# Kernel optimization log

Hardware: AMD Instinct MI355X
Metric: run time of the kernel (lower is better)

The kernel has to match this reference:

```python
import jax, jax.numpy as jnp
import numpy as np

HEADS = 2
C1 = 33    # per-head out channels, conv1
C2 = 550   # per-head out channels, conv2


def _lin_params(key, fan_in, fan_out):
    kw, kb = jax.random.split(key)
    scale = 1.0 / np.sqrt(fan_in)
    W = jax.random.uniform(kw, (fan_in, fan_out), jnp.float32, -scale, scale)
    b = jax.random.uniform(kb, (fan_out,), jnp.float32, -scale, scale)
    return W, b


def transformer_conv(x, src, dst, Wq, bq, Wk, bk, Wv, bv, Ws, bs, heads, out_ch):
    """PyG TransformerConv (concat=True, root_weight=True, beta=False)."""
    N = x.shape[0]
    q = (x @ Wq + bq).reshape(N, heads, out_ch)  # query of target node i
    k = (x @ Wk + bk).reshape(N, heads, out_ch)  # key of source node j
    v = (x @ Wv + bv).reshape(N, heads, out_ch)  # value of source node j
    # attention logits per edge: [E, H]
    alpha = jnp.einsum('ehc,ehc->eh', q[dst], k[src]) / jnp.sqrt(jnp.float32(out_ch))
    # segment softmax over incoming edges of each dst node
    m = jax.lax.stop_gradient(jax.ops.segment_max(alpha, dst, num_segments=N))  # [N,H]
    e = jnp.exp(alpha - m[dst])
    denom = jax.ops.segment_sum(e, dst, num_segments=N)  # [N,H]
    a = e / denom[dst]
    # weighted scatter-aggregate of source values: [N,H,C]
    out = jax.ops.segment_sum(a[..., None] * v[src], dst, num_segments=N)
    out = out.reshape(N, heads * out_ch)
    # root/skip connection
    out = out + x @ Ws + bs
    return out


def setup_inputs() -> dict:
    key = jax.random.key(0)
    ks = jax.random.split(key, 10)
    N, E, IN = 20000, 120000, 256
    x = jax.random.normal(ks[0], (N, IN), jnp.float32)
    edge_index = jax.random.randint(ks[1], (2, E), 0, N, jnp.int64 if jax.config.jax_enable_x64 else jnp.int32)
    d = {'x': x, 'edge_index': edge_index}
    # conv1: IN -> heads*C1
    d['Wq1'], d['bq1'] = _lin_params(ks[2], IN, HEADS * C1)
    d['Wk1'], d['bk1'] = _lin_params(ks[3], IN, HEADS * C1)
    d['Wv1'], d['bv1'] = _lin_params(ks[4], IN, HEADS * C1)
    d['Ws1'], d['bs1'] = _lin_params(ks[5], IN, HEADS * C1)
    # conv2: heads*C1 -> heads*C2
    IN2 = HEADS * C1
    d['Wq2'], d['bq2'] = _lin_params(ks[6], IN2, HEADS * C2)
    d['Wk2'], d['bk2'] = _lin_params(ks[7], IN2, HEADS * C2)
    d['Wv2'], d['bv2'] = _lin_params(ks[8], IN2, HEADS * C2)
    d['Ws2'], d['bs2'] = _lin_params(ks[9], IN2, HEADS * C2)
    return d


def reference(x, edge_index, Wq1, bq1, Wk1, bk1, Wv1, bv1, Ws1, bs1,
              Wq2, bq2, Wk2, bk2, Wv2, bv2, Ws2, bs2):
    src, dst = edge_index[0], edge_index[1]
    h = transformer_conv(x, src, dst, Wq1, bq1, Wk1, bk1, Wv1, bv1, Ws1, bs1, HEADS, C1)
    h = transformer_conv(h, src, dst, Wq2, bq2, Wk2, bk2, Wv2, bv2, Ws2, bs2, HEADS, C2)
    # x.view(N, 550, heads).max(dim=2) -- faithful to the original reshape layout
    h = h.reshape(h.shape[0], C2, HEADS)
    return jnp.max(h, axis=2)
```

## Files before the change

kernel.cpp:

```cpp
#include <hip/hip_runtime.h>
#include <math.h>

#define HEADS 2
#define C1    33
#define C2    550
#define D1    66
#define D2    1100
#define IN1   256
#define PROJW 288
#define KU    224
#define N2P   1152
#define KZ    96
#define ZW    144

typedef __attribute__((ext_vector_type(8))) short bfrag;
typedef __attribute__((ext_vector_type(4))) float f32x4;

__device__ inline unsigned short f2bf(float f) {
    unsigned int u = __float_as_uint(f);
    u += 0x7FFFu + ((u >> 16) & 1u);
    return (unsigned short)(u >> 16);
}

__device__ inline int xcd_slot(int bid, int slots) {
    return (bid >> 3) + (bid & 7) * slots;
}

__global__ void k_cvt(const float* __restrict__ x, unsigned short* __restrict__ xb, int total4) {
    int i = blockIdx.x * blockDim.x + threadIdx.x;
    if (i >= total4) return;
    float4 v = ((const float4*)x)[i];
    ushort4 o;
    o.x = f2bf(v.x); o.y = f2bf(v.y); o.z = f2bf(v.z); o.w = f2bf(v.w);
    ((ushort4*)xb)[i] = o;
}

__global__ void k_prep1(const float* __restrict__ Wq, const float* __restrict__ bq,
                        const float* __restrict__ Wk, const float* __restrict__ bk,
                        const float* __restrict__ Wv, const float* __restrict__ bv,
                        const float* __restrict__ Ws, const float* __restrict__ bs,
                        unsigned short* __restrict__ Wt1, float* __restrict__ bcat) {
    int bid = blockIdx.x;
    int lk = bid & 3, t = bid >> 2;
    int ks = t & 7, g = t >> 3;
    int col = threadIdx.x;
    int c = g * 96 + col;
    int k0 = ks * 32 + lk * 8;
    short vals[8];
    float bia = 0.f;
    if (c < 4 * D1) {
        int m = c / D1, j = c % D1;
        const float* W; const float* B;
        switch (m) {
            case 0: W = Wq; B = bq; break;
            case 1: W = Wk; B = bk; break;
            case 2: W = Wv; B = bv; break;
            default: W = Ws; B = bs; break;
        }
        #pragma unroll
        for (int e = 0; e < 8; e++) vals[e] = (short)f2bf(W[(size_t)(k0 + e) * D1 + j]);
        bia = B[j];
    } else {
        #pragma unroll
        for (int e = 0; e < 8; e++) vals[e] = 0;
    }
    *(bfrag*)&Wt1[((size_t)bid * 96 + col) * 8] = *(bfrag*)vals;
    if (ks == 0 && lk == 0) bcat[c] = bia;
}

__global__ void k_prep2(const float* __restrict__ Wv2, const float* __restrict__ bv2,
                        const float* __restrict__ Ws2, const float* __restrict__ bs2,
                        unsigned short* __restrict__ W2t,
                        float* __restrict__ bvp, float* __restrict__ bsp) {
    int bid = blockIdx.x;
    int lk = bid & 3, t = bid >> 2;
    int ks = t % 7, g = t / 7;
    int col = threadIdx.x;
    int c = g * 96 + col;
    int k0 = ks * 32 + lk * 8;
    short vals[8];
    #pragma unroll
    for (int e = 0; e < 8; e++) {
        int k = k0 + e;
        float val = 0.f;
        if (c < D2) {
            if (c < C2) {
                if (k < 66) val = Wv2[(size_t)k * D2 + c];
                else if (k >= 132 && k < 198) val = Ws2[(size_t)(k - 132) * D2 + c];
            } else {
                if (k >= 66 && k < 132) val = Wv2[(size_t)(k - 66) * D2 + c];
                else if (k >= 132 && k < 198) val = Ws2[(size_t)(k - 132) * D2 + c];
            }
        }
        vals[e] = (short)f2bf(val);
    }
    *(bfrag*)&W2t[((size_t)bid * 96 + col) * 8] = *(bfrag*)vals;
    if (ks == 0 && lk == 0) {
        bvp[c] = (c < D2) ? bv2[c] : 0.f;
        bsp[c] = (c < D2) ? bs2[c] : 0.f;
    }
}

__global__ void k_hist(const int* __restrict__ dst, int E, int* __restrict__ cnt) {
    int e = blockIdx.x * blockDim.x + threadIdx.x;
    if (e < E) atomicAdd(&cnt[dst[e]], 1);
}

__global__ void k_scan(const int* __restrict__ cnt, int* __restrict__ roff,
                       int* __restrict__ pos, int N) {
    __shared__ int wsum[16];
    __shared__ int carry_s;
    int tid = threadIdx.x, wid = tid >> 6, lane = tid & 63;
    if (tid == 0) { carry_s = 0; roff[0] = 0; }
    __syncthreads();
    for (int base = 0; base < N; base += 1024) {
        int i = base + tid;
        int v = (i < N) ? cnt[i] : 0;
        int x = v;
        #pragma unroll
        for (int s = 1; s < 64; s <<= 1) {
            int t = __shfl_up(x, s, 64);
            if (lane >= s) x += t;
        }
        if (lane == 63) wsum[wid] = x;
        __syncthreads();
        if (tid < 16) {
            int y = wsum[tid];
            #pragma unroll
            for (int s = 1; s < 16; s <<= 1) {
                int t = __shfl_up(y, s, 16);
                if (tid >= s) y += t;
            }
            wsum[tid] = y;
        }
        __syncthreads();
        int carry = carry_s;
        int incl = carry + (wid ? wsum[wid - 1] : 0) + x;
        if (i < N) { roff[i + 1] = incl; pos[i] = incl - v; }
        __syncthreads();
        if (tid == 0) carry_s = carry + wsum[15];
        __syncthreads();
    }
}

__global__ void k_fill(const int* __restrict__ src, const int* __restrict__ dst, int E,
                       int* __restrict__ pos, int* __restrict__ elist) {
    int e = blockIdx.x * blockDim.x + threadIdx.x;
    if (e < E) {
        int slot = atomicAdd(&pos[dst[e]], 1);
        elist[slot] = src[e];
    }
}

__global__ __launch_bounds__(256) void k_mm1(
        const unsigned short* __restrict__ A, const unsigned short* __restrict__ B,
        const float* __restrict__ bias, float* __restrict__ proj, int N,
        int nRow, int slots) {
    int s = xcd_slot(blockIdx.x, slots);
    if (s >= nRow * 3) return;
    int rowt = s / 3, g = s - rowt * 3;
    int cbase = g * 96;
    int wave = threadIdx.x >> 6, lane = threadIdx.x & 63;
    int lr = lane & 15, lk = lane >> 4;
    int rbase = rowt * 128 + wave * 32;
    int ar[2];
    #pragma unroll
    for (int mi = 0; mi < 2; mi++) {
        int r = rbase + mi * 16 + lr;
        ar[mi] = (r < N) ? r : (N - 1);
    }
    bfrag a[2][8];
    #pragma unroll
    for (int mi = 0; mi < 2; mi++)
        #pragma unroll
        for (int ks = 0; ks < 8; ks++)
            a[mi][ks] = *(const bfrag*)(A + (size_t)ar[mi] * IN1 + ks * 32 + lk * 8);
    f32x4 acc[2][6];
    #pragma unroll
    for (int mi = 0; mi < 2; mi++)
        #pragma unroll
        for (int ni = 0; ni < 6; ni++) acc[mi][ni] = (f32x4){0.f, 0.f, 0.f, 0.f};
    #pragma unroll
    for (int ks = 0; ks < 8; ks++) {
        bfrag b[6];
        #pragma unroll
        for (int ni = 0; ni < 6; ni++)
            b[ni] = *(const bfrag*)(B + (size_t)(g * 8 + ks) * 3072 + lk * 768 + (ni * 16 + lr) * 8);
        #pragma unroll
        for (int mi = 0; mi < 2; mi++)
            #pragma unroll
            for (int ni = 0; ni < 6; ni++)
                acc[mi][ni] = __builtin_amdgcn_mfma_f32_16x16x32_bf16(a[mi][ks], b[ni], acc[mi][ni], 0, 0, 0);
    }
    #pragma unroll
    for (int mi = 0; mi < 2; mi++) {
        #pragma unroll
        for (int ni = 0; ni < 6; ni++) {
            int col = cbase + ni * 16 + lr;
            float bia = bias[col];
            #pragma unroll
            for (int r = 0; r < 4; r++) {
                int row = rbase + mi * 16 + lk * 4 + r;
                if (row < N) proj[(size_t)row * PROJW + col] = acc[mi][ni][r] + bia;
            }
        }
    }
}

__global__ __launch_bounds__(128) void k_conv1(
        const float* __restrict__ proj, const int* __restrict__ roff,
        const int* __restrict__ elist, float* __restrict__ h1,
        unsigned short* __restrict__ h1b, int N) {
    int n = blockIdx.x;
    int h = threadIdx.x >> 6;
    int lane = threadIdx.x & 63;
    size_t pb = (size_t)n * PROJW;
    int hc = h * C1;
    bool ok = (lane < C1);
    float my_q = ok ? proj[pb + hc + lane] : 0.f;
    float s1v  = ok ? proj[pb + 198 + hc + lane] : 0.f;
    float m = -INFINITY, lsum = 0.f, acc = 0.f;
    int e0 = roff[n], e1 = roff[n + 1];
    const float isc = 0.17407765595569785f;
    int e = e0;
    for (; e + 3 < e1; e += 4) {
        int s0 = elist[e], s1 = elist[e + 1], s2 = elist[e + 2], s3 = elist[e + 3];
        size_t b0 = (size_t)s0 * PROJW, b1 = (size_t)s1 * PROJW;
        size_t b2 = (size_t)s2 * PROJW, b3 = (size_t)s3 * PROJW;
        float k0 = ok ? proj[b0 + 66 + hc + lane] : 0.f;
        float k1 = ok ? proj[b1 + 66 + hc + lane] : 0.f;
        float k2 = ok ? proj[b2 + 66 + hc + lane] : 0.f;
        float k3 = ok ? proj[b3 + 66 + hc + lane] : 0.f;
        float v0 = ok ? proj[b0 + 132 + hc + lane] : 0.f;
        float v1 = ok ? proj[b1 + 132 + hc + lane] : 0.f;
        float v2 = ok ? proj[b2 + 132 + hc + lane] : 0.f;
        float v3 = ok ? proj[b3 + 132 + hc + lane] : 0.f;
        float p0 = my_q * k0, p1 = my_q * k1, p2 = my_q * k2, p3 = my_q * k3;
        #pragma unroll
        for (int off = 32; off >= 1; off >>= 1) {
            p0 += __shfl_xor(p0, off, 64);
            p1 += __shfl_xor(p1, off, 64);
            p2 += __shfl_xor(p2, off, 64);
            p3 += __shfl_xor(p3, off, 64);
        }
        float a0 = p0 * isc, a1 = p1 * isc, a2 = p2 * isc, a3 = p3 * isc;
        float mp = fmaxf(fmaxf(a0, a1), fmaxf(a2, a3));
        float e0v = __expf(a0 - mp), e1v = __expf(a1 - mp);
        float e2v = __expf(a2 - mp), e3v = __expf(a3 - mp);
        float lp = (e0v + e1v) + (e2v + e3v);
        float ap = (e0v * v0 + e1v * v1) + (e2v * v2 + e3v * v3);
        float mnew = fmaxf(m, mp);
        float sc = __expf(m - mnew), sp = __expf(mp - mnew);
        lsum = lsum * sc + lp * sp;
        acc  = acc * sc + ap * sp;
        m = mnew;
    }
    for (; e + 1 < e1; e += 2) {
        int sa = elist[e], sb = elist[e + 1];
        size_t ba = (size_t)sa * PROJW, bb = (size_t)sb * PROJW;
        float ka = ok ? proj[ba + 66 + hc + lane] : 0.f;
        float va = ok ? proj[ba + 132 + hc + lane] : 0.f;
        float kb = ok ? proj[bb + 66 + hc + lane] : 0.f;
        float vb = ok ? proj[bb + 132 + hc + lane] : 0.f;
        float pa = my_q * ka, pbv = my_q * kb;
        #pragma unroll
        for (int off = 32; off >= 1; off >>= 1) {
            pa  += __shfl_xor(pa, off, 64);
            pbv += __shfl_xor(pbv, off, 64);
        }
        float aa = pa * isc, ab = pbv * isc;
        float mp = fmaxf(aa, ab);
        float ea = __expf(aa - mp), eb = __expf(ab - mp);
        float lp = ea + eb, ap = ea * va + eb * vb;
        float mnew = fmaxf(m, mp);
        float sc = __expf(m - mnew), sp = __expf(mp - mnew);
        lsum = lsum * sc + lp * sp;
        acc  = acc * sc + ap * sp;
        m = mnew;
    }
    if (e < e1) {
        int s = elist[e];
        size_t sb = (size_t)s * PROJW;
        float kv = ok ? proj[sb + 66 + hc + lane] : 0.f;
        float vv = ok ? proj[sb + 132 + hc + lane] : 0.f;
        float prod = my_q * kv;
        #pragma unroll
        for (int off = 32; off >= 1; off >>= 1) prod += __shfl_xor(prod, off, 64);
        float alpha = prod * isc;
        float mnew = fmaxf(m, alpha);
        float sc = __expf(m - mnew);
        float p = __expf(alpha - mnew);
        lsum = lsum * sc + p;
        acc  = acc * sc + p * vv;
        m = mnew;
    }
    if (ok) {
        float res = (lsum > 0.f) ? acc / lsum : 0.f;
        float val = res + s1v;
        h1[(size_t)n * D1 + hc + lane] = val;
        h1b[(size_t)n * KZ + hc + lane] = f2bf(val);
    } else if (h == 1 && lane >= C1 && lane < C1 + 30) {
        h1b[(size_t)n * KZ + D1 + (lane - C1)] = 0;
    }
}

__global__ __launch_bounds__(256) void k_precomp(
        const float* __restrict__ Wq2, const float* __restrict__ bq2,
        const float* __restrict__ Wk2, const float* __restrict__ bk2,
        float* __restrict__ G, float* __restrict__ wqbk,
        float* __restrict__ wkbq, float* __restrict__ cc) {
    int wave = threadIdx.x >> 6, lane = threadIdx.x & 63;
    int j = blockIdx.x * 4 + wave;
    if (j >= 8978) return;
    const float *u, *v;
    float* outp;
    if (j < 8976) {
        int h = j / 4488;
        int r = j % 4488;
        int a = r / 68, b = r % 68;
        if (b < 66)      { u = Wq2 + (size_t)a * D2 + h * C2; v = Wk2 + (size_t)b * D2 + h * C2; outp = &G[h * 4356 + a * 66 + b]; }
        else if (b == 66){ u = Wq2 + (size_t)a * D2 + h * C2; v = bk2 + h * C2;                  outp = &wqbk[h * 66 + a]; }
        else             { u = Wk2 + (size_t)a * D2 + h * C2; v = bq2 + h * C2;                  outp = &wkbq[h * 66 + a]; }
    } else {
        int h = j - 8976;
        u = bq2 + h * C2; v = bk2 + h * C2; outp = &cc[h];
    }
    float acc = 0.f;
    for (int c = lane; c < C2; c += 64) acc += u[c] * v[c];
    #pragma unroll
    for (int off = 32; off >= 1; off >>= 1) acc += __shfl_xor(acc, off, 64);
    if (lane == 0) *outp = acc;
}

__global__ void k_prepz(const float* __restrict__ G, const float* __restrict__ wqbk,
                        const float* __restrict__ wkbq, unsigned short* __restrict__ GBt) {
    int bid = blockIdx.x;
    int lk = bid & 3, t = bid >> 2;
    int ks = t % 3, g = t / 3;
    int col = threadIdx.x;
    int r = g * 96 + col;
    int k0 = ks * 32 + lk * 8;
    short vals[8];
    #pragma unroll
    for (int e = 0; e < 8; e++) {
        int k = k0 + e;
        float v = 0.f;
        if (k < D1) {
            if (r < 132) v = G[r * D1 + k];
            else if (r < 134) v = wqbk[(r - 132) * D1 + k];
            else if (r < 136) v = wkbq[(r - 134) * D1 + k];
        }
        vals[e] = (short)f2bf(v);
    }
    *(bfrag*)&GBt[((size_t)bid * 96 + col) * 8] = *(bfrag*)vals;
}

__global__ __launch_bounds__(256) void k_mmz(
        const unsigned short* __restrict__ A, const unsigned short* __restrict__ B,
        float* __restrict__ Z, int N, int nRow, int slots) {
    int s = xcd_slot(blockIdx.x, slots);
    if (s >= nRow * 2) return;
    int rowt = s >> 1, g = s & 1;
    int wave = threadIdx.x >> 6, lane = threadIdx.x & 63;
    int lr = lane & 15, lk = lane >> 4;
    int rbase = rowt * 64 + (wave >> 1) * 32;
    int ch = (wave & 1) * 48;
    int cbase = g * 96 + ch;
    f32x4 acc[2][3];
    #pragma unroll
    for (int i = 0; i < 2; i++)
        #pragma unroll
        for (int j = 0; j < 3; j++) acc[i][j] = (f32x4){0.f, 0.f, 0.f, 0.f};
    int ar[2];
    #pragma unroll
    for (int mi = 0; mi < 2; mi++) {
        int r = rbase + mi * 16 + lr;
        ar[mi] = (r < N) ? r : (N - 1);
    }
    #pragma unroll
    for (int ks = 0; ks < 3; ks++) {
        bfrag a[2], b[3];
        #pragma unroll
        for (int mi = 0; mi < 2; mi++)
            a[mi] = *(const bfrag*)(A + (size_t)ar[mi] * KZ + ks * 32 + lk * 8);
        #pragma unroll
        for (int ni = 0; ni < 3; ni++)
            b[ni] = *(const bfrag*)(B + (size_t)(g * 3 + ks) * 3072 + lk * 768 + (ch + ni * 16 + lr) * 8);
        #pragma unroll
        for (int mi = 0; mi < 2; mi++)
            #pragma unroll
            for (int ni = 0; ni < 3; ni++)
                acc[mi][ni] = __builtin_amdgcn_mfma_f32_16x16x32_bf16(a[mi], b[ni], acc[mi][ni], 0, 0, 0);
    }
    #pragma unroll
    for (int mi = 0; mi < 2; mi++) {
        #pragma unroll
        for (int ni = 0; ni < 3; ni++) {
            int col = cbase + ni * 16 + lr;
            if (col >= 136) continue;
            #pragma unroll
            for (int r = 0; r < 4; r++) {
                int row = rbase + mi * 16 + lk * 4 + r;
                if (row < N) Z[(size_t)row * ZW + col] = acc[mi][ni][r];
            }
        }
    }
}

__global__ __launch_bounds__(128) void k_conv2(
        const float* __restrict__ h1, const float* __restrict__ Z,
        const float* __restrict__ cc, const int* __restrict__ roff,
        const int* __restrict__ elist, unsigned short* __restrict__ U,
        float* __restrict__ flag, int N) {
    int n = blockIdx.x;
    int h = threadIdx.x >> 6;
    int lane = threadIdx.x & 63;
    int c0 = lane, c1 = lane + 64;
    bool ok1 = (c1 < D1);
    float hd0 = h1[(size_t)n * D1 + c0];
    float hd1 = ok1 ? h1[(size_t)n * D1 + c1] : 0.f;
    float adv = Z[(size_t)n * ZW + 132 + h] + cc[h];
    float m = -INFINITY, lsum = 0.f, a0 = 0.f, a1 = 0.f;
    int e0 = roff[n], e1 = roff[n + 1];
    const float isc = 0.04264014327112209f;
    int hD = h * D1;
    int e = e0;
    for (; e + 3 < e1; e += 4) {
        int s0 = elist[e], s1 = elist[e + 1], s2 = elist[e + 2], s3 = elist[e + 3];
        const float* z0 = Z + (size_t)s0 * ZW;
        const float* z1 = Z + (size_t)s1 * ZW;
        const float* z2 = Z + (size_t)s2 * ZW;
        const float* z3 = Z + (size_t)s3 * ZW;
        float p0 = hd0 * z0[hD + c0] + (ok1 ? hd1 * z0[hD + c1] : 0.f);
        float p1 = hd0 * z1[hD + c0] + (ok1 ? hd1 * z1[hD + c1] : 0.f);
        float p2 = hd0 * z2[hD + c0] + (ok1 ? hd1 * z2[hD + c1] : 0.f);
        float p3 = hd0 * z3[hD + c0] + (ok1 ? hd1 * z3[hD + c1] : 0.f);
        #pragma unroll
        for (int off = 32; off >= 1; off >>= 1) {
            p0 += __shfl_xor(p0, off, 64);
            p1 += __shfl_xor(p1, off, 64);
            p2 += __shfl_xor(p2, off, 64);
            p3 += __shfl_xor(p3, off, 64);
        }
        float al0 = (p0 + adv + z0[134 + h]) * isc;
        float al1 = (p1 + adv + z1[134 + h]) * isc;
        float al2 = (p2 + adv + z2[134 + h]) * isc;
        float al3 = (p3 + adv + z3[134 + h]) * isc;
        float va00 = h1[(size_t)s0 * D1 + c0];
        float va01 = ok1 ? h1[(size_t)s0 * D1 + c1] : 0.f;
        float va10 = h1[(size_t)s1 * D1 + c0];
        float va11 = ok1 ? h1[(size_t)s1 * D1 + c1] : 0.f;
        float va20 = h1[(size_t)s2 * D1 + c0];
        float va21 = ok1 ? h1[(size_t)s2 * D1 + c1] : 0.f;
        float va30 = h1[(size_t)s3 * D1 + c0];
        float va31 = ok1 ? h1[(size_t)s3 * D1 + c1] : 0.f;
        float mp = fmaxf(fmaxf(al0, al1), fmaxf(al2, al3));
        float e0v = __expf(al0 - mp), e1v = __expf(al1 - mp);
        float e2v = __expf(al2 - mp), e3v = __expf(al3 - mp);
        float lp = (e0v + e1v) + (e2v + e3v);
        float ap0 = (e0v * va00 + e1v * va10) + (e2v * va20 + e3v * va30);
        float ap1 = (e0v * va01 + e1v * va11) + (e2v * va21 + e3v * va31);
        float mnew = fmaxf(m, mp);
        float sc = __expf(m - mnew), sp = __expf(mp - mnew);
        lsum = lsum * sc + lp * sp;
        a0 = a0 * sc + ap0 * sp;
        a1 = a1 * sc + ap1 * sp;
        m = mnew;
    }
    for (; e + 1 < e1; e += 2) {
        int sa = elist[e], sb = elist[e + 1];
        const float* za = Z + (size_t)sa * ZW;
        const float* zb = Z + (size_t)sb * ZW;
        float pa = hd0 * za[hD + c0] + (ok1 ? hd1 * za[hD + c1] : 0.f);
        float pb = hd0 * zb[hD + c0] + (ok1 ? hd1 * zb[hD + c1] : 0.f);
        #pragma unroll
        for (int off = 32; off >= 1; off >>= 1) {
            pa += __shfl_xor(pa, off, 64);
            pb += __shfl_xor(pb, off, 64);
        }
        float aa = (pa + adv + za[134 + h]) * isc;
        float ab = (pb + adv + zb[134 + h]) * isc;
        float va0 = h1[(size_t)sa * D1 + c0];
        float va1 = ok1 ? h1[(size_t)sa * D1 + c1] : 0.f;
        float vb0 = h1[(size_t)sb * D1 + c0];
        float vb1 = ok1 ? h1[(size_t)sb * D1 + c1] : 0.f;
        float mp = fmaxf(aa, ab);
        float ea = __expf(aa - mp), eb = __expf(ab - mp);
        float lp = ea + eb;
        float ap0 = ea * va0 + eb * vb0;
        float ap1 = ea * va1 + eb * vb1;
        float mnew = fmaxf(m, mp);
        float sc = __expf(m - mnew), sp = __expf(mp - mnew);
        lsum = lsum * sc + lp * sp;
        a0 = a0 * sc + ap0 * sp;
        a1 = a1 * sc + ap1 * sp;
        m = mnew;
    }
    if (e < e1) {
        int s = elist[e];
        const float* zr = Z + (size_t)s * ZW;
        float prod = hd0 * zr[hD + c0] + (ok1 ? hd1 * zr[hD + c1] : 0.f);
        #pragma unroll
        for (int off = 32; off >= 1; off >>= 1) prod += __shfl_xor(prod, off, 64);
        float alpha = (prod + adv + zr[134 + h]) * isc;
        float mnew = fmaxf(m, alpha);
        float sc = __expf(m - mnew);
        float p = __expf(alpha - mnew);
        lsum = lsum * sc + p;
        float v0 = h1[(size_t)s * D1 + c0];
        float vv1 = ok1 ? h1[(size_t)s * D1 + c1] : 0.f;
        a0 = a0 * sc + p * v0;
        a1 = a1 * sc + p * vv1;
        m = mnew;
    }
    float inv = (lsum > 0.f) ? 1.f / lsum : 0.f;
    size_t ub = (size_t)n * KU;
    U[ub + hD + c0] = f2bf(a0 * inv);
    if (ok1) U[ub + hD + c1] = f2bf(a1 * inv);
    if (h == 0) {
        U[ub + 132 + c0] = f2bf(hd0);
        if (ok1) U[ub + 132 + c1] = f2bf(hd1);
    } else if (lane < KU - 198) {
        U[ub + 198 + lane] = 0;
    }
    if (lane == 0) flag[n * 2 + h] = (lsum > 0.f) ? 1.f : 0.f;
}

__global__ __launch_bounds__(256) void k_mm2(
        const unsigned short* __restrict__ A, const unsigned short* __restrict__ B,
        const float* __restrict__ bvp, const float* __restrict__ bsp,
        const float* __restrict__ flag, float* __restrict__ out, int N,
        int nRow, int slots) {
    int s = xcd_slot(blockIdx.x, slots);
    if (s >= nRow * 12) return;
    int rowt = s / 12, g = s - rowt * 12;
    int cbase = g * 96;
    int wave = threadIdx.x >> 6, lane = threadIdx.x & 63;
    int lr = lane & 15, lk = lane >> 4;
    int rbase = rowt * 128 + wave * 32;
    int ar[2];
    #pragma unroll
    for (int mi = 0; mi < 2; mi++) {
        int r = rbase + mi * 16 + lr;
        ar[mi] = (r < N) ? r : (N - 1);
    }
    bfrag a[2][7];
    #pragma unroll
    for (int mi = 0; mi < 2; mi++)
        #pragma unroll
        for (int ks = 0; ks < 7; ks++)
            a[mi][ks] = *(const bfrag*)(A + (size_t)ar[mi] * KU + ks * 32 + lk * 8);
    f32x4 acc[2][6];
    #pragma unroll
    for (int mi = 0; mi < 2; mi++)
        #pragma unroll
        for (int ni = 0; ni < 6; ni++) acc[mi][ni] = (f32x4){0.f, 0.f, 0.f, 0.f};
    #pragma unroll
    for (int ks = 0; ks < 7; ks++) {
        bfrag b[6];
        #pragma unroll
        for (int ni = 0; ni < 6; ni++)
            b[ni] = *(const bfrag*)(B + (size_t)(g * 7 + ks) * 3072 + lk * 768 + (ni * 16 + lr) * 8);
        #pragma unroll
        for (int mi = 0; mi < 2; mi++)
            #pragma unroll
            for (int ni = 0; ni < 6; ni++)
                acc[mi][ni] = __builtin_amdgcn_mfma_f32_16x16x32_bf16(a[mi][ks], b[ni], acc[mi][ni], 0, 0, 0);
    }
    #pragma unroll
    for (int mi = 0; mi < 2; mi++) {
        #pragma unroll
        for (int ni = 0; ni < 6; ni++) {
            int col = cbase + ni * 16 + lr;
            float bv = bvp[col], bs_ = bsp[col];
            int hh = (col >= C2) ? 1 : 0;
            #pragma unroll
            for (int r = 0; r < 4; r++) {
                int row = rbase + mi * 16 + lk * 4 + r;
                int fr = (row < N) ? row : 0;
                float val = acc[mi][ni][r] + flag[fr * 2 + hh] * bv + bs_;
                float oth = __shfl_xor(val, 1, 64);
                if (row < N && col < D2 && !(col & 1))
                    out[(size_t)row * C2 + (col >> 1)] = fmaxf(val, oth);
            }
        }
    }
}

extern "C" void kernel_launch(void* const* d_in, const int* in_sizes, int n_in,
                              void* d_out, int out_size, void* d_ws, size_t ws_size,
                              hipStream_t stream) {
    const float* x  = (const float*)d_in[0];
    const int*   ei = (const int*)d_in[1];
    int N = in_sizes[0] / IN1;
    int E = in_sizes[1] / 2;
    const int* src = ei;
    const int* dst = ei + E;

    const float *Wq1 = (const float*)d_in[2],  *bq1 = (const float*)d_in[3];
    const float *Wk1 = (const float*)d_in[4],  *bk1 = (const float*)d_in[5];
    const float *Wv1 = (const float*)d_in[6],  *bv1 = (const float*)d_in[7];
    const float *Ws1 = (const float*)d_in[8],  *bs1 = (const float*)d_in[9];
    const float *Wq2 = (const float*)d_in[10], *bq2 = (const float*)d_in[11];
    const float *Wk2 = (const float*)d_in[12], *bk2 = (const float*)d_in[13];
    const float *Wv2 = (const float*)d_in[14], *bv2 = (const float*)d_in[15];
    const float *Ws2 = (const float*)d_in[16], *bs2 = (const float*)d_in[17];

    char* w = (char*)d_ws;
    size_t off = 0;
    auto take = [&](size_t bytes) { size_t o = off; off = (off + bytes + 255) & ~(size_t)255; return o; };

    unsigned short* xb = (unsigned short*)(w + take((size_t)N * IN1 * 2));
    size_t proj_off = take((size_t)N * PROJW * 4);
    float* proj = (float*)(w + proj_off);
    float* Z = proj;
    unsigned short* U = (unsigned short*)(w + proj_off + (size_t)N * ZW * 4);
    float* h1   = (float*)(w + take((size_t)N * D1 * 4));
    unsigned short* h1b = (unsigned short*)(w + take((size_t)N * KZ * 2));
    float* flag = (float*)(w + take((size_t)N * 2 * 4));
    float* G    = (float*)(w + take((size_t)2 * D1 * D1 * 4));
    float* wqbk = (float*)(w + take(2 * D1 * 4));
    float* wkbq = (float*)(w + take(2 * D1 * 4));
    float* cc   = (float*)(w + take(2 * 4));
    unsigned short* GBt = (unsigned short*)(w + take((size_t)24 * 96 * 8 * 2));
    unsigned short* Wt1 = (unsigned short*)(w + take((size_t)96 * 96 * 8 * 2));
    float* bcat = (float*)(w + take(PROJW * 4));
    unsigned short* W2t = (unsigned short*)(w + take((size_t)336 * 96 * 8 * 2));
    float* bvp  = (float*)(w + take(N2P * 4));
    float* bsp  = (float*)(w + take(N2P * 4));
    int* cnt   = (int*)(w + take((size_t)N * 4));
    int* roff  = (int*)(w + take((size_t)(N + 1) * 4));
    int* pos   = (int*)(w + take((size_t)N * 4));
    int* elist = (int*)(w + take((size_t)E * 4));

    hipMemsetAsync(cnt, 0, (size_t)N * sizeof(int), stream);
    k_hist<<<(E + 255) / 256, 256, 0, stream>>>(dst, E, cnt);
    k_scan<<<1, 1024, 0, stream>>>(cnt, roff, pos, N);
    k_fill<<<(E + 255) / 256, 256, 0, stream>>>(src, dst, E, pos, elist);

    k_cvt<<<(N * IN1 / 4 + 255) / 256, 256, 0, stream>>>(x, xb, N * IN1 / 4);
    k_prep1<<<96, 96, 0, stream>>>(Wq1, bq1, Wk1, bk1, Wv1, bv1, Ws1, bs1, Wt1, bcat);
    k_prep2<<<336, 96, 0, stream>>>(Wv2, bv2, Ws2, bs2, W2t, bvp, bsp);
    k_precomp<<<(8978 + 3) / 4, 256, 0, stream>>>(Wq2, bq2, Wk2, bk2, G, wqbk, wkbq, cc);
    k_prepz<<<24, 96, 0, stream>>>(G, wqbk, wkbq, GBt);

    int nRow1 = (N + 127) / 128;
    int tot1  = nRow1 * 3;
    int slots1 = (tot1 + 7) / 8;
    int nRowZ = (N + 63) / 64;
    int totZ  = nRowZ * 2;
    int slotsZ = (totZ + 7) / 8;
    int nRow2 = (N + 127) / 128;
    int tot2  = nRow2 * 12;
    int slots2 = (tot2 + 7) / 8;

    k_mm1<<<slots1 * 8, 256, 0, stream>>>(xb, Wt1, bcat, proj, N, nRow1, slots1);
    k_conv1<<<N, 128, 0, stream>>>(proj, roff, elist, h1, h1b, N);

    k_mmz<<<slotsZ * 8, 256, 0, stream>>>(h1b, GBt, Z, N, nRowZ, slotsZ);

    k_conv2<<<N, 128, 0, stream>>>(h1, Z, cc, roff, elist, U, flag, N);

    k_mm2<<<slots2 * 8, 256, 0, stream>>>(U, W2t, bvp, bsp, flag, (float*)d_out, N, nRow2, slots2);
}
```

Before: 192.5 us.

## Fold conv2 biases into padded K columns and stage mm2 output through LDS

The value and skip biases of the second layer move into spare K rows of the packed weight matrix. Matching indicator columns are written into U: a per-head flag for rows that have incoming edges, plus a constant one. This removes the separate flag buffer and the per-element bias loads from the mm2 epilogue. The epilogue now writes the head-max results into shared memory and stores them as contiguous row segments, replacing scattered strided stores. Biases now pass through bf16 rounding, which adds a little precision loss.

```diff
diff --git a/kernel.cpp b/kernel.cpp
--- a/kernel.cpp
+++ b/kernel.cpp
@@ -70,8 +70,7 @@
 
 __global__ void k_prep2(const float* __restrict__ Wv2, const float* __restrict__ bv2,
                         const float* __restrict__ Ws2, const float* __restrict__ bs2,
-                        unsigned short* __restrict__ W2t,
-                        float* __restrict__ bvp, float* __restrict__ bsp) {
+                        unsigned short* __restrict__ W2t) {
     int bid = blockIdx.x;
     int lk = bid & 3, t = bid >> 2;
     int ks = t % 7, g = t / 7;
@@ -87,18 +86,18 @@
             if (c < C2) {
                 if (k < 66) val = Wv2[(size_t)k * D2 + c];
                 else if (k >= 132 && k < 198) val = Ws2[(size_t)(k - 132) * D2 + c];
+                else if (k == 198) val = bv2[c];
+                else if (k == 223) val = bs2[c];
             } else {
                 if (k >= 66 && k < 132) val = Wv2[(size_t)(k - 66) * D2 + c];
                 else if (k >= 132 && k < 198) val = Ws2[(size_t)(k - 132) * D2 + c];
+                else if (k == 199) val = bv2[c];
+                else if (k == 223) val = bs2[c];
             }
         }
         vals[e] = (short)f2bf(val);
     }
     *(bfrag*)&W2t[((size_t)bid * 96 + col) * 8] = *(bfrag*)vals;
-    if (ks == 0 && lk == 0) {
-        bvp[c] = (c < D2) ? bv2[c] : 0.f;
-        bsp[c] = (c < D2) ? bs2[c] : 0.f;
-    }
 }
 
 __global__ void k_hist(const int* __restrict__ dst, int E, int* __restrict__ cnt) {
@@ -410,8 +409,7 @@
 __global__ __launch_bounds__(128) void k_conv2(
         const float* __restrict__ h1, const float* __restrict__ Z,
         const float* __restrict__ cc, const int* __restrict__ roff,
-        const int* __restrict__ elist, unsigned short* __restrict__ U,
-        float* __restrict__ flag, int N) {
+        const int* __restrict__ elist, unsigned short* __restrict__ U, int N) {
     int n = blockIdx.x;
     int h = threadIdx.x >> 6;
     int lane = threadIdx.x & 63;
@@ -517,24 +515,23 @@
     size_t ub = (size_t)n * KU;
     U[ub + hD + c0] = f2bf(a0 * inv);
     if (ok1) U[ub + hD + c1] = f2bf(a1 * inv);
+    if (lane == 0) U[ub + 198 + h] = (lsum > 0.f) ? (unsigned short)0x3F80 : (unsigned short)0;
     if (h == 0) {
         U[ub + 132 + c0] = f2bf(hd0);
         if (ok1) U[ub + 132 + c1] = f2bf(hd1);
-    } else if (lane < KU - 198) {
-        U[ub + 198 + lane] = 0;
-    }
-    if (lane == 0) flag[n * 2 + h] = (lsum > 0.f) ? 1.f : 0.f;
+        if (lane == 1) U[ub + 223] = (unsigned short)0x3F80;
+    } else if (lane >= 34 && lane < 57) {
+        U[ub + 200 + (lane - 34)] = 0;
+    }
 }
 
 __global__ __launch_bounds__(256) void k_mm2(
         const unsigned short* __restrict__ A, const unsigned short* __restrict__ B,
-        const float* __restrict__ bvp, const float* __restrict__ bsp,
-        const float* __restrict__ flag, float* __restrict__ out, int N,
-        int nRow, int slots) {
+        float* __restrict__ out, int N, int nRow, int slots) {
+    __shared__ float ot[4][32][49];
     int s = xcd_slot(blockIdx.x, slots);
     if (s >= nRow * 12) return;
     int rowt = s / 12, g = s - rowt * 12;
-    int cbase = g * 96;
     int wave = threadIdx.x >> 6, lane = threadIdx.x & 63;
     int lr = lane & 15, lk = lane >> 4;
     int rbase = rowt * 128 + wave * 32;
@@ -571,19 +568,25 @@
     for (int mi = 0; mi < 2; mi++) {
         #pragma unroll
         for (int ni = 0; ni < 6; ni++) {
-            int col = cbase + ni * 16 + lr;
-            float bv = bvp[col], bs_ = bsp[col];
-            int hh = (col >= C2) ? 1 : 0;
             #pragma unroll
             for (int r = 0; r < 4; r++) {
-                int row = rbase + mi * 16 + lk * 4 + r;
-                int fr = (row < N) ? row : 0;
-                float val = acc[mi][ni][r] + flag[fr * 2 + hh] * bv + bs_;
+                float val = acc[mi][ni][r];
                 float oth = __shfl_xor(val, 1, 64);
-                if (row < N && col < D2 && !(col & 1))
-                    out[(size_t)row * C2 + (col >> 1)] = fmaxf(val, oth);
+                if (!(lane & 1))
+                    ot[wave][mi * 16 + lk * 4 + r][ni * 8 + (lr >> 1)] = fmaxf(val, oth);
             }
         }
+    }
+    __syncthreads();
+    int colb = g * 48;
+    #pragma unroll
+    for (int i = 0; i < 24; i++) {
+        int t = i * 64 + lane;
+        int r32 = t / 48, pos = t - r32 * 48;
+        int row = rbase + r32;
+        int col = colb + pos;
+        if (row < N && col < C2)
+            out[(size_t)row * C2 + col] = ot[wave][r32][pos];
     }
 }
 
@@ -617,7 +620,6 @@
     unsigned short* U = (unsigned short*)(w + proj_off + (size_t)N * ZW * 4);
     float* h1   = (float*)(w + take((size_t)N * D1 * 4));
     unsigned short* h1b = (unsigned short*)(w + take((size_t)N * KZ * 2));
-    float* flag = (float*)(w + take((size_t)N * 2 * 4));
     float* G    = (float*)(w + take((size_t)2 * D1 * D1 * 4));
     float* wqbk = (float*)(w + take(2 * D1 * 4));
     float* wkbq = (float*)(w + take(2 * D1 * 4));
@@ -626,8 +628,6 @@
     unsigned short* Wt1 = (unsigned short*)(w + take((size_t)96 * 96 * 8 * 2));
     float* bcat = (float*)(w + take(PROJW * 4));
     unsigned short* W2t = (unsigned short*)(w + take((size_t)336 * 96 * 8 * 2));
-    float* bvp  = (float*)(w + take(N2P * 4));
-    float* bsp  = (float*)(w + take(N2P * 4));
     int* cnt   = (int*)(w + take((size_t)N * 4));
     int* roff  = (int*)(w + take((size_t)(N + 1) * 4));
     int* pos   = (int*)(w + take((size_t)N * 4));
@@ -640,7 +640,7 @@
 
     k_cvt<<<(N * IN1 / 4 + 255) / 256, 256, 0, stream>>>(x, xb, N * IN1 / 4);
     k_prep1<<<96, 96, 0, stream>>>(Wq1, bq1, Wk1, bk1, Wv1, bv1, Ws1, bs1, Wt1, bcat);
-    k_prep2<<<336, 96, 0, stream>>>(Wv2, bv2, Ws2, bs2, W2t, bvp, bsp);
+    k_prep2<<<336, 96, 0, stream>>>(Wv2, bv2, Ws2, bs2, W2t);
     k_precomp<<<(8978 + 3) / 4, 256, 0, stream>>>(Wq2, bq2, Wk2, bk2, G, wqbk, wkbq, cc);
     k_prepz<<<24, 96, 0, stream>>>(G, wqbk, wkbq, GBt);
 
@@ -659,7 +659,7 @@
 
     k_mmz<<<slotsZ * 8, 256, 0, stream>>>(h1b, GBt, Z, N, nRowZ, slotsZ);
 
-    k_conv2<<<N, 128, 0, stream>>>(h1, Z, cc, roff, elist, U, flag, N);
-
-    k_mm2<<<slots2 * 8, 256, 0, stream>>>(U, W2t, bvp, bsp, flag, (float*)d_out, N, nRow2, slots2);
-}
+    k_conv2<<<N, 128, 0, stream>>>(h1, Z, cc, roff, elist, U, N);
+
+    k_mm2<<<slots2 * 8, 256, 0, stream>>>(U, W2t, (float*)d_out, N, nRow2, slots2);
+}
```

New measurement: 174.8 us. 9.2% less time.
